# Kernel tuning notes

Measured on AMD Instinct MI355X. Metric: run time of the kernel, lower is better.

Reference implementation:

```python
import jax, jax.numpy as jnp
import numpy as np

N_NODES = 50000


def setup_inputs() -> dict:
    key = jax.random.key(0)
    k1, k2, k3, k4, k5 = jax.random.split(key, 5)
    feature = jax.random.normal(k1, (N_NODES, 128), dtype=jnp.float32)
    src = jax.random.randint(k2, (1600000,), 0, N_NODES, dtype=jnp.int32)
    dst = jax.random.randint(k3, (1600000,), 0, N_NODES, dtype=jnp.int32)
    W = jax.random.normal(k4, (128, 128), dtype=jnp.float32) * (1.0 / np.sqrt(128))
    b = jax.random.normal(k5, (128,), dtype=jnp.float32) * 0.01
    return {"feature": feature, "src": src, "dst": dst, "W": W, "b": b}


def reference(feature, src, dst, W, b):
    # DGL update_all(copy_src('h','m'), sum('m','h')):
    # for each edge (u -> v): message m = h[u]; node v accumulates sum of incoming messages.
    msgs = feature[src]  # [E, F] gather
    h = jax.ops.segment_sum(msgs, dst, num_segments=N_NODES)  # [N, F] scatter-add
    # nn.Linear(in_feats, out_feats): h @ W.T + b
    return h @ W.T + b
```

## Files before the change

kernel.cpp:

```cpp
#include <hip/hip_runtime.h>

#define F      128
#define RSH    5
#define RNODES 32
#define NBUCK  1563
#define CB     1280
#define CH     8192
#define OVCAP  65536
#define G_PART 196

typedef __attribute__((ext_vector_type(8))) short short8;
typedef __attribute__((ext_vector_type(8))) unsigned short ushort8v;
typedef __attribute__((ext_vector_type(4))) float f32x4;

__device__ inline short f2bf(float f) {
  unsigned u = __float_as_uint(f);
  u += 0x7fff + ((u >> 16) & 1);
  return (short)(u >> 16);
}
__device__ inline float bf2f(unsigned short u) {
  return __uint_as_float((unsigned)u << 16);
}

__global__ __launch_bounds__(512) void k_fused(
    const float* __restrict__ X, const float* __restrict__ W,
    const int* __restrict__ src, const int* __restrict__ dst,
    unsigned short* __restrict__ Yb,
    unsigned* __restrict__ pk, unsigned* __restrict__ gcur,
    unsigned* __restrict__ ovcnt, unsigned long long* __restrict__ ovlist,
    int N, int E, int nTiles) {
  __shared__ unsigned smem[14444];
  const int t = threadIdx.x;

  if (blockIdx.x < G_PART) {
    unsigned* lpk   = smem;
    unsigned* cnt   = smem + CH;
    unsigned* offs  = cnt + NBUCK;
    unsigned* cur   = offs + NBUCK;
    unsigned* gbase = cur + NBUCK;
    const int nchunk = (E + CH - 1) / CH;

    for (int c = blockIdx.x; c < nchunk; c += G_PART) {
      const int e0   = c * CH;
      const int ecnt = min(CH, E - e0);

      for (int i = t; i < NBUCK; i += 512) cnt[i] = 0;
      __syncthreads();

      for (int i = t; i < ecnt; i += 512)
        atomicAdd(&cnt[(unsigned)dst[e0 + i] >> RSH], 1u);
      __syncthreads();

      unsigned lv0, lv1, lv2, lv3;
      {
        const int i0 = t * 4;
        lv0 = (i0 + 0 < NBUCK) ? cnt[i0 + 0] : 0;
        lv1 = (i0 + 1 < NBUCK) ? cnt[i0 + 1] : 0;
        lv2 = (i0 + 2 < NBUCK) ? cnt[i0 + 2] : 0;
        lv3 = (i0 + 3 < NBUCK) ? cnt[i0 + 3] : 0;
      }
      cur[t] = lv0 + lv1 + lv2 + lv3;
      __syncthreads();
      for (int d2 = 1; d2 < 512; d2 <<= 1) {
        const unsigned add = (t >= d2) ? cur[t - d2] : 0;
        __syncthreads();
        cur[t] += add;
        __syncthreads();
      }
      unsigned ebase = (t > 0) ? cur[t - 1] : 0;
      __syncthreads();
      {
        const int i0 = t * 4;
        if (i0 + 0 < NBUCK) { offs[i0 + 0] = ebase; cur[i0 + 0] = ebase; ebase += lv0; }
        if (i0 + 1 < NBUCK) { offs[i0 + 1] = ebase; cur[i0 + 1] = ebase; ebase += lv1; }
        if (i0 + 2 < NBUCK) { offs[i0 + 2] = ebase; cur[i0 + 2] = ebase; ebase += lv2; }
        if (i0 + 3 < NBUCK) { offs[i0 + 3] = ebase; cur[i0 + 3] = ebase; ebase += lv3; }
      }
      __syncthreads();

      for (int i = t; i < ecnt; i += 512) {
        const unsigned d = (unsigned)dst[e0 + i];
        const unsigned b = d >> RSH;
        const unsigned p = atomicAdd(&cur[b], 1u);
        lpk[p] = (unsigned)src[e0 + i] | ((d & (RNODES - 1)) << 16) | (b << 21);
      }
      __syncthreads();

      for (int i = t; i < NBUCK; i += 512)
        if (cnt[i] > 0)
          gbase[i] = (unsigned)i * CB + atomicAdd(&gcur[i], cnt[i]);
      __syncthreads();

      for (int p = t; p < ecnt; p += 512) {
        const unsigned v = lpk[p];
        const unsigned b = v >> 21;
        const unsigned idx = gbase[b] + ((unsigned)p - offs[b]);
        if (idx < (b + 1) * (unsigned)CB) {
          pk[idx] = v & 0x1FFFFFu;
        } else {
          const unsigned o = atomicAdd(ovcnt, 1u);
          if (o < OVCAP) {
            const unsigned s  = v & 0xFFFFu;
            const unsigned dl = (v >> 16) & (RNODES - 1);
            ovlist[o] = ((unsigned long long)(b * RNODES + dl) << 32) | s;
          }
        }
      }
      __syncthreads();
    }
  } else {
    short* Wp = (short*)smem;
    for (int fid = t; fid < 2048; fid += 512) {
      const int lane = fid & 63;
      const int c    = (fid >> 6) & 3;
      const int jt   = fid >> 8;
      const int j    = jt * 16 + (lane & 15);
      const int k0   = c * 32 + (lane >> 4) * 8;
      short8 s;
      #pragma unroll
      for (int i = 0; i < 8; ++i) s[i] = f2bf(W[j * F + k0 + i]);
      *reinterpret_cast<short8*>(Wp + fid * 8) = s;
    }
    __syncthreads();

    const int lane = t & 63;
    const int tile = (blockIdx.x - G_PART) * 8 + (t >> 6);
    if (tile >= nTiles) return;
    const int row0 = tile * 16;
    const int r    = row0 + (lane & 15);
    const int k0   = (lane >> 4) * 8;

    short8 a[4];
    #pragma unroll
    for (int c = 0; c < 4; ++c) {
      if (r < N) {
        const float* p = X + (size_t)r * F + c * 32 + k0;
        const float4 x0 = *reinterpret_cast<const float4*>(p);
        const float4 x1 = *reinterpret_cast<const float4*>(p + 4);
        a[c][0] = f2bf(x0.x); a[c][1] = f2bf(x0.y);
        a[c][2] = f2bf(x0.z); a[c][3] = f2bf(x0.w);
        a[c][4] = f2bf(x1.x); a[c][5] = f2bf(x1.y);
        a[c][6] = f2bf(x1.z); a[c][7] = f2bf(x1.w);
      } else {
        #pragma unroll
        for (int i = 0; i < 8; ++i) a[c][i] = 0;
      }
    }

    #pragma unroll
    for (int jt = 0; jt < 8; ++jt) {
      f32x4 acc = {0.f, 0.f, 0.f, 0.f};
      #pragma unroll
      for (int c = 0; c < 4; ++c) {
        const short8 bfrag = *reinterpret_cast<const short8*>(
            Wp + ((jt * 4 + c) * 64 + lane) * 8);
        acc = __builtin_amdgcn_mfma_f32_16x16x32_bf16(a[c], bfrag, acc, 0, 0, 0);
      }
      const int col   = jt * 16 + (lane & 15);
      const int rbase = row0 + (lane >> 4) * 4;
      #pragma unroll
      for (int reg = 0; reg < 4; ++reg)
        if (rbase + reg < N)
          Yb[(size_t)(rbase + reg) * F + col] = (unsigned short)f2bf(acc[reg]);
    }
  }
}

__global__ __launch_bounds__(512) void k_reduce2(
    const unsigned short* __restrict__ Yb,
    const unsigned* __restrict__ pk,
    const unsigned* __restrict__ gcur,
    const float* __restrict__ b,
    float* __restrict__ out,
    int N) {
  __shared__ unsigned s_pk[CB];
  __shared__ unsigned short s_src[CB];
  __shared__ unsigned lcnt[RNODES], loffs[RNODES], lcur[RNODES];
  const int bkt = blockIdx.x;
  const int t = threadIdx.x;
  const unsigned base = (unsigned)bkt * CB;
  const unsigned m = min(gcur[bkt], (unsigned)CB);

  for (unsigned i = t; i < m; i += 512) s_pk[i] = pk[base + i];
  if (t < RNODES) lcnt[t] = 0;
  __syncthreads();
  for (unsigned i = t; i < m; i += 512)
    atomicAdd(&lcnt[s_pk[i] >> 16], 1u);
  __syncthreads();
  if (t == 0) {
    unsigned r = 0;
    #pragma unroll
    for (int i = 0; i < RNODES; ++i) { loffs[i] = r; lcur[i] = r; r += lcnt[i]; }
  }
  __syncthreads();
  for (unsigned i = t; i < m; i += 512) {
    const unsigned v = s_pk[i];
    const unsigned p = atomicAdd(&lcur[v >> 16], 1u);
    s_src[p] = (unsigned short)(v & 0xFFFFu);
  }
  __syncthreads();

  const int lane = t & 63;
  const int g    = lane >> 4;
  const int q    = lane & 15;
  const int dl   = (t >> 6) * 4 + g;
  const int v    = bkt * RNODES + dl;
  const int deg  = (int)lcnt[dl];
  const int off  = (int)loffs[dl];

  float acc[8];
  #pragma unroll
  for (int j = 0; j < 8; ++j) acc[j] = 0.f;

  int k = 0;
  for (; k + 3 < deg; k += 4) {
    int sid[4];
    #pragma unroll
    for (int u = 0; u < 4; ++u) sid[u] = (int)s_src[off + k + u];
    ushort8v y[4];
    #pragma unroll
    for (int u = 0; u < 4; ++u)
      y[u] = *reinterpret_cast<const ushort8v*>(
          Yb + (size_t)sid[u] * F + q * 8);
    #pragma unroll
    for (int j = 0; j < 8; ++j)
      acc[j] += (bf2f(y[0][j]) + bf2f(y[1][j])) +
                (bf2f(y[2][j]) + bf2f(y[3][j]));
  }
  for (; k < deg; ++k) {
    const int s0 = (int)s_src[off + k];
    const ushort8v y = *reinterpret_cast<const ushort8v*>(
        Yb + (size_t)s0 * F + q * 8);
    #pragma unroll
    for (int j = 0; j < 8; ++j) acc[j] += bf2f(y[j]);
  }

  if (v < N) {
    float* op = out + (size_t)v * F + q * 8;
    const float4 b0 = *reinterpret_cast<const float4*>(b + q * 8);
    const float4 b1 = *reinterpret_cast<const float4*>(b + q * 8 + 4);
    float4 o0 = make_float4(acc[0] + b0.x, acc[1] + b0.y,
                            acc[2] + b0.z, acc[3] + b0.w);
    float4 o1 = make_float4(acc[4] + b1.x, acc[5] + b1.y,
                            acc[6] + b1.z, acc[7] + b1.w);
    *reinterpret_cast<float4*>(op)     = o0;
    *reinterpret_cast<float4*>(op + 4) = o1;
  }
}

__global__ __launch_bounds__(256) void k_overflow(
    const unsigned* __restrict__ ovcnt,
    const unsigned long long* __restrict__ ovlist,
    const unsigned short* __restrict__ Yb,
    float* __restrict__ out, int N) {
  const unsigned n = min(*ovcnt, (unsigned)OVCAP);
  const int lane = threadIdx.x & 63;
  const int w  = (int)((blockIdx.x * blockDim.x + threadIdx.x) >> 6);
  const int nw = (int)((gridDim.x * blockDim.x) >> 6);
  for (unsigned i = w; i < n; i += nw) {
    const unsigned long long e = ovlist[i];
    const unsigned s = (unsigned)(e & 0xFFFFFFFFu);
    const unsigned d = (unsigned)(e >> 32);
    const float x0 = bf2f(Yb[(size_t)s * F + lane * 2]);
    const float x1 = bf2f(Yb[(size_t)s * F + lane * 2 + 1]);
    unsafeAtomicAdd(&out[(size_t)d * F + lane * 2],     x0);
    unsafeAtomicAdd(&out[(size_t)d * F + lane * 2 + 1], x1);
  }
}

extern "C" void kernel_launch(void* const* d_in, const int* in_sizes, int n_in,
                              void* d_out, int out_size, void* d_ws, size_t ws_size,
                              hipStream_t stream) {
  const float* feat = (const float*)d_in[0];
  const int*   src  = (const int*)d_in[1];
  const int*   dst  = (const int*)d_in[2];
  const float* W    = (const float*)d_in[3];
  const float* b    = (const float*)d_in[4];
  float*       out  = (float*)d_out;

  const int N = in_sizes[0] / F;
  const int E = in_sizes[1];

  char* w = (char*)d_ws;
  auto alloc = [&](size_t bytes) {
    char* p = w; w += (bytes + 255) & ~(size_t)255; return p;
  };
  unsigned short*     Yb      = (unsigned short*)alloc((size_t)N * F * 2);
  unsigned*           pk      = (unsigned*)alloc((size_t)NBUCK * CB * 4);
  unsigned*           gcur    = (unsigned*)alloc((size_t)(NBUCK + 1) * 4);
  unsigned*           ovcnt   = gcur + NBUCK;
  unsigned long long* ovlist  = (unsigned long long*)alloc((size_t)OVCAP * 8);

  hipMemsetAsync(gcur, 0, (size_t)(NBUCK + 1) * 4, stream);

  const int nTiles = (N + 15) / 16;
  const int gGemm  = (nTiles + 7) / 8;
  k_fused<<<G_PART + gGemm, 512, 0, stream>>>(
      feat, W, src, dst, Yb, pk, gcur, ovcnt, ovlist, N, E, nTiles);

  k_reduce2<<<NBUCK, 512, 0, stream>>>(Yb, pk, gcur, b, out, N);

  k_overflow<<<16, 256, 0, stream>>>(ovcnt, ovlist, Yb, out, N);
}
```

Measured before the change: 84.69 us.

## Split reduce over two feature halves and reuse count array for global bases

```diff
diff --git a/kernel.cpp b/kernel.cpp
--- a/kernel.cpp
+++ b/kernel.cpp
@@ -10,7 +10,6 @@
 #define G_PART 196
 
 typedef __attribute__((ext_vector_type(8))) short short8;
-typedef __attribute__((ext_vector_type(8))) unsigned short ushort8v;
 typedef __attribute__((ext_vector_type(4))) float f32x4;
 
 __device__ inline short f2bf(float f) {
@@ -29,7 +28,7 @@
     unsigned* __restrict__ pk, unsigned* __restrict__ gcur,
     unsigned* __restrict__ ovcnt, unsigned long long* __restrict__ ovlist,
     int N, int E, int nTiles) {
-  __shared__ unsigned smem[14444];
+  __shared__ unsigned smem[CH + 3 * NBUCK];
   const int t = threadIdx.x;
 
   if (blockIdx.x < G_PART) {
@@ -37,7 +36,6 @@
     unsigned* cnt   = smem + CH;
     unsigned* offs  = cnt + NBUCK;
     unsigned* cur   = offs + NBUCK;
-    unsigned* gbase = cur + NBUCK;
     const int nchunk = (E + CH - 1) / CH;
 
     for (int c = blockIdx.x; c < nchunk; c += G_PART) {
@@ -86,15 +84,16 @@
       }
       __syncthreads();
 
-      for (int i = t; i < NBUCK; i += 512)
-        if (cnt[i] > 0)
-          gbase[i] = (unsigned)i * CB + atomicAdd(&gcur[i], cnt[i]);
+      for (int i = t; i < NBUCK; i += 512) {
+        const unsigned c0 = cnt[i];
+        if (c0 > 0) cnt[i] = (unsigned)i * CB + atomicAdd(&gcur[i], c0);
+      }
       __syncthreads();
 
       for (int p = t; p < ecnt; p += 512) {
         const unsigned v = lpk[p];
         const unsigned b = v >> 21;
-        const unsigned idx = gbase[b] + ((unsigned)p - offs[b]);
+        const unsigned idx = cnt[b] + ((unsigned)p - offs[b]);
         if (idx < (b + 1) * (unsigned)CB) {
           pk[idx] = v & 0x1FFFFFu;
         } else {
@@ -176,7 +175,8 @@
   __shared__ unsigned s_pk[CB];
   __shared__ unsigned short s_src[CB];
   __shared__ unsigned lcnt[RNODES], loffs[RNODES], lcur[RNODES];
-  const int bkt = blockIdx.x;
+  const int bkt = blockIdx.x % NBUCK;
+  const int s   = blockIdx.x / NBUCK;
   const int t = threadIdx.x;
   const unsigned base = (unsigned)bkt * CB;
   const unsigned m = min(gcur[bkt], (unsigned)CB);
@@ -207,44 +207,41 @@
   const int v    = bkt * RNODES + dl;
   const int deg  = (int)lcnt[dl];
   const int off  = (int)loffs[dl];
-
-  float acc[8];
+  const unsigned short* Yh = Yb + s * 64;
+
+  float acc[4];
   #pragma unroll
-  for (int j = 0; j < 8; ++j) acc[j] = 0.f;
+  for (int j = 0; j < 4; ++j) acc[j] = 0.f;
 
   int k = 0;
   for (; k + 3 < deg; k += 4) {
     int sid[4];
     #pragma unroll
     for (int u = 0; u < 4; ++u) sid[u] = (int)s_src[off + k + u];
-    ushort8v y[4];
+    ushort4 y[4];
     #pragma unroll
     for (int u = 0; u < 4; ++u)
-      y[u] = *reinterpret_cast<const ushort8v*>(
-          Yb + (size_t)sid[u] * F + q * 8);
-    #pragma unroll
-    for (int j = 0; j < 8; ++j)
-      acc[j] += (bf2f(y[0][j]) + bf2f(y[1][j])) +
-                (bf2f(y[2][j]) + bf2f(y[3][j]));
+      y[u] = *reinterpret_cast<const ushort4*>(
+          Yh + (size_t)sid[u] * F + q * 4);
+    acc[0] += (bf2f(y[0].x) + bf2f(y[1].x)) + (bf2f(y[2].x) + bf2f(y[3].x));
+    acc[1] += (bf2f(y[0].y) + bf2f(y[1].y)) + (bf2f(y[2].y) + bf2f(y[3].y));
+    acc[2] += (bf2f(y[0].z) + bf2f(y[1].z)) + (bf2f(y[2].z) + bf2f(y[3].z));
+    acc[3] += (bf2f(y[0].w) + bf2f(y[1].w)) + (bf2f(y[2].w) + bf2f(y[3].w));
   }
   for (; k < deg; ++k) {
     const int s0 = (int)s_src[off + k];
-    const ushort8v y = *reinterpret_cast<const ushort8v*>(
-        Yb + (size_t)s0 * F + q * 8);
-    #pragma unroll
-    for (int j = 0; j < 8; ++j) acc[j] += bf2f(y[j]);
+    const ushort4 y = *reinterpret_cast<const ushort4*>(
+        Yh + (size_t)s0 * F + q * 4);
+    acc[0] += bf2f(y.x); acc[1] += bf2f(y.y);
+    acc[2] += bf2f(y.z); acc[3] += bf2f(y.w);
   }
 
   if (v < N) {
-    float* op = out + (size_t)v * F + q * 8;
-    const float4 b0 = *reinterpret_cast<const float4*>(b + q * 8);
-    const float4 b1 = *reinterpret_cast<const float4*>(b + q * 8 + 4);
-    float4 o0 = make_float4(acc[0] + b0.x, acc[1] + b0.y,
-                            acc[2] + b0.z, acc[3] + b0.w);
-    float4 o1 = make_float4(acc[4] + b1.x, acc[5] + b1.y,
-                            acc[6] + b1.z, acc[7] + b1.w);
-    *reinterpret_cast<float4*>(op)     = o0;
-    *reinterpret_cast<float4*>(op + 4) = o1;
+    const int j = s * 64 + q * 4;
+    const float4 bb = *reinterpret_cast<const float4*>(b + j);
+    float4 o = make_float4(acc[0] + bb.x, acc[1] + bb.y,
+                           acc[2] + bb.z, acc[3] + bb.w);
+    *reinterpret_cast<float4*>(out + (size_t)v * F + j) = o;
   }
 }
 
@@ -298,7 +295,7 @@
   k_fused<<<G_PART + gGemm, 512, 0, stream>>>(
       feat, W, src, dst, Yb, pk, gcur, ovcnt, ovlist, N, E, nTiles);
 
-  k_reduce2<<<NBUCK, 512, 0, stream>>>(Yb, pk, gcur, b, out, N);
+  k_reduce2<<<2 * NBUCK, 512, 0, stream>>>(Yb, pk, gcur, b, out, N);
 
   k_overflow<<<16, 256, 0, stream>>>(ovcnt, ovlist, Yb, out, N);
 }
```

Result: faster. 82.06 us (-3.1%).
